# Optimization experiments

Measured on AMD Instinct MI355X. Metric: run time of the kernel, lower is better.

Reference implementation:

```python
import jax, jax.numpy as jnp
import numpy as np

S, T, B = 32, 48, 1024      # src_len, tgt_len, batch
E, H = 256, 1024            # embedding, hidden
VS, VT = 256, 256           # source/target vocab


def setup_inputs() -> dict:
    key = jax.random.key(0)
    ks = jax.random.split(key, 20)
    s = 0.02
    n = jax.random.normal
    inp = {
        "src": jax.random.randint(ks[0], (S, B), 0, VS),
        "tgt": jax.random.randint(ks[1], (T, B), 0, VT),
        "enc_emb": n(ks[2], (VS, E), jnp.float32) * s,
        "enc_Wih0": n(ks[3], (4 * H, E), jnp.float32) * s,
        "enc_Whh0": n(ks[4], (4 * H, H), jnp.float32) * s,
        "enc_b0": jnp.zeros((4 * H,), jnp.float32),
        "enc_Wih1": n(ks[5], (4 * H, H), jnp.float32) * s,
        "enc_Whh1": n(ks[6], (4 * H, H), jnp.float32) * s,
        "enc_b1": jnp.zeros((4 * H,), jnp.float32),
        "dec_emb": n(ks[7], (VT, E), jnp.float32) * s,
        "dec_Wih0": n(ks[8], (4 * H, E), jnp.float32) * s,
        "dec_Whh0": n(ks[9], (4 * H, H), jnp.float32) * s,
        "dec_b0": jnp.zeros((4 * H,), jnp.float32),
        "dec_Wih1": n(ks[10], (4 * H, H), jnp.float32) * s,
        "dec_Whh1": n(ks[11], (4 * H, H), jnp.float32) * s,
        "dec_b1": jnp.zeros((4 * H,), jnp.float32),
        "fc_W": n(ks[12], (H, VT), jnp.float32) * s,
        "fc_b": jnp.zeros((VT,), jnp.float32),
    }
    return inp


def lstm_step(x, h, c, Wih, Whh, b):
    # PyTorch gate order: i, f, g, o
    z = x @ Wih.T + h @ Whh.T + b
    i, f, g, o = jnp.split(z, 4, axis=-1)
    c = jax.nn.sigmoid(f) * c + jax.nn.sigmoid(i) * jnp.tanh(g)
    h = jax.nn.sigmoid(o) * jnp.tanh(c)
    return h, c


def run_layer(xs, Wih, Whh, b):
    # xs: [S, B, in]; returns all hidden states and final (h, c)
    bsz = xs.shape[1]
    h0 = jnp.zeros((bsz, Whh.shape[1]), xs.dtype)

    def step(carry, x):
        h, c = lstm_step(x, carry[0], carry[1], Wih, Whh, b)
        return (h, c), h

    (h, c), hs = jax.lax.scan(step, (h0, h0), xs)
    return hs, h, c


def reference(src, tgt, enc_emb, enc_Wih0, enc_Whh0, enc_b0, enc_Wih1, enc_Whh1,
              enc_b1, dec_emb, dec_Wih0, dec_Whh0, dec_b0, dec_Wih1, dec_Whh1,
              dec_b1, fc_W, fc_b):
    # ---- Encoder: 2-layer LSTM over source ----
    xe = enc_emb[src]                                   # [S, B, E]
    hs0, h0, c0 = run_layer(xe, enc_Wih0, enc_Whh0, enc_b0)
    _, h1, c1 = run_layer(hs0, enc_Wih1, enc_Whh1, enc_b1)

    # ---- Decoder: per-timestep loop, teacher forcing ratio = 1.0 ----
    def dec_step(carry, tok):
        dh0, dc0, dh1, dc1 = carry
        x = dec_emb[tok]                                # [B, E]
        dh0, dc0 = lstm_step(x, dh0, dc0, dec_Wih0, dec_Whh0, dec_b0)
        dh1, dc1 = lstm_step(dh0, dh1, dc1, dec_Wih1, dec_Whh1, dec_b1)
        logits = dh1 @ fc_W + fc_b                      # [B, VT]
        return (dh0, dc0, dh1, dc1), logits

    _, logits = jax.lax.scan(dec_step, (h0, c0, h1, c1), tgt[:-1])  # [T-1, B, VT]
    # outputs[0] is never written in the original -> stays zeros
    out = jnp.concatenate([jnp.zeros((1,) + logits.shape[1:], logits.dtype), logits], axis=0)
    return out
```

## Files before the change

kernel.cpp:

```cpp
#include <hip/hip_runtime.h>
#include <hip/hip_fp16.h>

typedef __attribute__((ext_vector_type(8))) short short8;
typedef __attribute__((ext_vector_type(4))) float floatx4;

#define DEVFN static __device__ __forceinline__

DEVFN short f2h(float v) { return __half_as_short(__float2half(v)); }

DEVFN void gload16(const void* g, void* l) {
  void* gnc = const_cast<void*>(g);
  __builtin_amdgcn_global_load_lds(
      (__attribute__((address_space(1))) void*)gnc,
      (__attribute__((address_space(3))) void*)l, 16, 0, 0);
}

DEVFN unsigned* fset(unsigned* f, int role, int s, int gy) {
  return f + ((((role * 79) + s) * 8 + gy) << 5);
}

__global__ __launch_bounds__(256, 2) void pers_kernel(
    short* xe0, short* xe1, short* xd0, short* xd1,
    const short* wc_e0, const short* wc_e1, const short* wc_d0, const short* wc_d1,
    const float* eb0, const float* eb1, const float* db0, const float* db1,
    const short* embe, const short* embd,
    const int* __restrict__ src, const int* __restrict__ tgt,
    short* dh1, unsigned* flags) {
  __shared__ short smem[32768];
  const int tid = threadIdx.x;
  const int lane = tid & 63;
  const int wv = tid >> 6;
  const int wm = wv >> 1;
  const int wu = wv & 1;
  const int l15 = lane & 15;
  const int l4 = lane >> 4;
  const int bid = blockIdx.x;
  const int xcd = bid & 7;
  const int idx = bid >> 3;
  const int role1 = idx >> 5;
  const int rem = idx & 31;
  const int ut = xcd * 4 + (rem >> 3);
  const int gy = rem & 7;
  const int u0 = ut * 32;
  const int m0 = gy * 128;
  const int srow = lane >> 3;
  const int swseg = ((lane & 7) * 16) ^ (srow * 16);
  const long SL0 = 1024l * 1280, SL1 = 1024l * 2048;

  float cst[16];
#pragma unroll
  for (int i = 0; i < 16; ++i) cst[i] = 0.f;

  for (int s = 0; s < 79; ++s) {
    unsigned* WA = nullptr;
    unsigned* WB = nullptr;
    if (!role1) {
      if (s >= 1) WA = fset(flags, 0, s - 1, gy);
      if (s >= 3) WB = fset(flags, 1, s - 3, gy);
    } else {
      WA = fset(flags, 0, s, gy);
      if (s >= 1) WB = fset(flags, 1, s - 1, gy);
    }
    if (WA || WB) {
      if (tid < 64) {
        unsigned* p = (tid < 32) ? (WA ? WA + tid : nullptr)
                                 : (WB ? WB + (tid - 32) : nullptr);
        if (p) {
          while (__hip_atomic_load(p, __ATOMIC_RELAXED,
                                   __HIP_MEMORY_SCOPE_AGENT) == 0u)
            __builtin_amdgcn_s_sleep(1);
          (void)__hip_atomic_load(p, __ATOMIC_ACQUIRE, __HIP_MEMORY_SCOPE_AGENT);
        }
      }
      __syncthreads();
    }

    const int enc = (s < 32) ? 1 : 0;
    const int t = enc ? s : s - 32;
    const int cur = t % 3, nxt = (t + 1) % 3;
    const short* A; const short* Wt; const float* bs; int ktot;
    short *d1 = nullptr, *d2 = nullptr, *d3 = nullptr, *xq = nullptr;
    int s1 = 0, o1 = 0, xs = 0;
    const short* xe = nullptr; const int* tk = nullptr;
    if (!role1) {
      if (enc) {
        A = xe0 + cur * SL0; Wt = wc_e0; bs = eb0; ktot = 1280;
        d2 = xe1 + cur * SL1;
        s1 = 1280; o1 = 256; xs = 1280;
        if (t < 31) { d1 = xe0 + nxt * SL0; xq = d1; xe = embe; tk = src + (t + 1) * 1024; }
        else        { d1 = xd0;             xq = xd0; xe = embd; tk = tgt; }
      } else {
        A = xd0 + cur * SL0; Wt = wc_d0; bs = db0; ktot = 1280;
        d1 = xd0 + nxt * SL0; s1 = 1280; o1 = 256;
        d2 = xd1 + cur * SL1;
        if (t < 46) { xq = xd0 + nxt * SL0; xs = 1280; xe = embd; tk = tgt + (t + 1) * 1024; }
      }
    } else {
      if (enc) {
        A = xe1 + cur * SL1; Wt = wc_e1; bs = eb1; ktot = 2048;
        d1 = (t < 31) ? (xe1 + nxt * SL1) : xd1; s1 = 2048; o1 = 1024;
      } else {
        A = xd1 + cur * SL1; Wt = wc_d1; bs = db1; ktot = 2048;
        d1 = xd1 + nxt * SL1; s1 = 2048; o1 = 1024;
        d3 = dh1 + (long)t * 1024 * 1024;
      }
    }

    floatx4 acc[4][4];
#pragma unroll
    for (int g = 0; g < 4; ++g)
#pragma unroll
      for (int mi = 0; mi < 4; ++mi) acc[g][mi] = (floatx4){0.f, 0.f, 0.f, 0.f};

    const char* Ab = (const char*)A;
    const char* Wb = (const char*)Wt;
    const long kbytes = (long)ktot * 2;
    const int nkb = ktot >> 6;

    auto stage = [&](int kb, int bufi) {
      const long kboff = (long)kb * 128;
      short* sb = smem + bufi * 16384;
#pragma unroll
      for (int ci = 0; ci < 8; ++ci) {
        const int c = wv * 8 + ci;
        void* lds = (void*)(sb + c * 512);
        if (c < 16) {
          const int row = c * 8 + srow;
          gload16(Ab + (long)(m0 + row) * kbytes + kboff + swseg, lds);
        } else {
          const int cb = c - 16;
          const int wrow = (cb >> 2) * 1024 + u0 + (cb & 3) * 8 + srow;
          gload16(Wb + (long)wrow * kbytes + kboff + swseg, lds);
        }
      }
    };

    stage(0, 0);
    __syncthreads();
    int buf = 0;
    for (int kb = 0; kb < nkb; ++kb) {
      if (kb + 1 < nkb) stage(kb + 1, buf ^ 1);
      const short* sb = smem + buf * 16384;
#pragma unroll
      for (int k0 = 0; k0 < 64; k0 += 32) {
        short8 fa[4];
        short8 fb[4];
#pragma unroll
        for (int mi = 0; mi < 4; ++mi) {
          const int r = wm * 64 + mi * 16 + l15;
          fa[mi] = *(const short8*)(sb + r * 64 + ((k0 + l4 * 8) ^ ((r & 7) << 3)));
        }
        {
          const int r = wu * 16 + l15;
          const int kk = (k0 + l4 * 8) ^ ((r & 7) << 3);
#pragma unroll
          for (int g = 0; g < 4; ++g)
            fb[g] = *(const short8*)(sb + 8192 + (g * 32 + r) * 64 + kk);
        }
#pragma unroll
        for (int g = 0; g < 4; ++g)
#pragma unroll
          for (int mi = 0; mi < 4; ++mi)
            asm volatile("v_mfma_f32_16x16x32_f16 %0, %1, %2, %0"
                         : "+v"(acc[g][mi])
                         : "v"(fa[mi]), "v"(fb[g]));
      }
      __syncthreads();
      buf ^= 1;
    }
    asm volatile("s_nop 7\ns_nop 7\ns_nop 7");

    const int u = u0 + wu * 16 + l15;
    const float bi = bs[u];
    const float bf_ = bs[1024 + u];
    const float bg = bs[2048 + u];
    const float bo = bs[3072 + u];
    short* ht = smem;
    const int uloc = wu * 16 + l15;
#pragma unroll
    for (int mi = 0; mi < 4; ++mi) {
#pragma unroll
      for (int j = 0; j < 4; ++j) {
        const float zi = acc[0][mi][j] + bi;
        const float zf = acc[1][mi][j] + bf_;
        const float zg = acc[2][mi][j] + bg;
        const float zo = acc[3][mi][j] + bo;
        const float gi = 1.f / (1.f + expf(-zi));
        const float gf = 1.f / (1.f + expf(-zf));
        const float gg = tanhf(zg);
        const float go = 1.f / (1.f + expf(-zo));
        const float cn = gf * cst[mi * 4 + j] + gi * gg;
        cst[mi * 4 + j] = cn;
        const int rl = wm * 64 + mi * 16 + l4 * 4 + j;
        ht[rl * 40 + uloc] = f2h(go * tanhf(cn));
      }
    }
    __syncthreads();

    {
      const int rl = tid >> 1;
      const int seg = (tid & 1) * 16;
      const short8 v0 = *(const short8*)(ht + rl * 40 + seg);
      const short8 v1 = *(const short8*)(ht + rl * 40 + seg + 8);
      const long col = u0 + seg;
      if (d1) {
        short* p = d1 + (long)(m0 + rl) * s1 + o1 + col;
        *(short8*)p = v0; *(short8*)(p + 8) = v1;
      }
      if (d2) {
        short* p = d2 + (long)(m0 + rl) * 2048 + col;
        *(short8*)p = v0; *(short8*)(p + 8) = v1;
      }
      if (d3) {
        short* p = d3 + (long)(m0 + rl) * 1024 + col;
        *(short8*)p = v0; *(short8*)(p + 8) = v1;
      }
    }
    if (xq && tid < 128) {
      const int i = ut * 128 + tid;
      const int row = i >> 5;
      const int e8 = (i & 31) * 8;
      const int b = m0 + row;
      const int tok = tk[b];
      const short8 v = *(const short8*)(xe + (long)tok * 256 + e8);
      *(short8*)(xq + (long)b * xs + e8) = v;
    }

    __syncthreads();
    if (tid == 0)
      __hip_atomic_store(fset(flags, role1, s, gy) + ut, 1u,
                         __ATOMIC_RELEASE, __HIP_MEMORY_SCOPE_AGENT);
  }
}

__global__ __launch_bounds__(256) void fc_kernel(
    const short* __restrict__ A, const short* __restrict__ W,
    const float* __restrict__ bias, float* __restrict__ outp) {
  __shared__ short smem[32768];
  const int tid = threadIdx.x;
  const int lane = tid & 63;
  const int wv = tid >> 6;
  const int wm = wv >> 1;
  const int wu = wv & 1;
  const int l15 = lane & 15;
  const int l4 = lane >> 4;
  const int u0 = blockIdx.x * 128;
  const int m0 = blockIdx.y * 128;
  const int srow = lane >> 3;
  const int swseg = ((lane & 7) * 16) ^ (srow * 16);

  floatx4 acc[4][4];
#pragma unroll
  for (int g = 0; g < 4; ++g)
#pragma unroll
    for (int mi = 0; mi < 4; ++mi) acc[g][mi] = (floatx4){0.f, 0.f, 0.f, 0.f};

  const char* Ab = (const char*)A;
  const char* Wb = (const char*)W;
  const long kbytes = 2048;
  const int nkb = 16;

  auto stage = [&](int kb, int bufi) {
    const long kboff = (long)kb * 128;
    short* sb = smem + bufi * 16384;
#pragma unroll
    for (int ci = 0; ci < 8; ++ci) {
      const int c = wv * 8 + ci;
      void* lds = (void*)(sb + c * 512);
      if (c < 16) {
        const int row = c * 8 + srow;
        gload16(Ab + (long)(m0 + row) * kbytes + kboff + swseg, lds);
      } else {
        const int cb = c - 16;
        const int wrow = (cb >> 2) * 32 + u0 + (cb & 3) * 8 + srow;
        gload16(Wb + (long)wrow * kbytes + kboff + swseg, lds);
      }
    }
  };

  stage(0, 0);
  __syncthreads();
  int buf = 0;
  for (int kb = 0; kb < nkb; ++kb) {
    if (kb + 1 < nkb) stage(kb + 1, buf ^ 1);
    const short* sb = smem + buf * 16384;
#pragma unroll
    for (int k0 = 0; k0 < 64; k0 += 32) {
      short8 fa[4];
      short8 fb[4];
#pragma unroll
      for (int mi = 0; mi < 4; ++mi) {
        const int r = wm * 64 + mi * 16 + l15;
        fa[mi] = *(const short8*)(sb + r * 64 + ((k0 + l4 * 8) ^ ((r & 7) << 3)));
      }
      {
        const int r = wu * 16 + l15;
        const int kk = (k0 + l4 * 8) ^ ((r & 7) << 3);
#pragma unroll
        for (int g = 0; g < 4; ++g)
          fb[g] = *(const short8*)(sb + 8192 + (g * 32 + r) * 64 + kk);
      }
#pragma unroll
      for (int g = 0; g < 4; ++g)
#pragma unroll
        for (int mi = 0; mi < 4; ++mi)
          asm volatile("v_mfma_f32_16x16x32_f16 %0, %1, %2, %0"
                       : "+v"(acc[g][mi])
                       : "v"(fa[mi]), "v"(fb[g]));
    }
    __syncthreads();
    buf ^= 1;
  }
  asm volatile("s_nop 7\ns_nop 7\ns_nop 7");

#pragma unroll
  for (int g = 0; g < 4; ++g) {
    const int n = u0 + g * 32 + wu * 16 + l15;
    const float bb = bias[n];
#pragma unroll
    for (int mi = 0; mi < 4; ++mi) {
#pragma unroll
      for (int j = 0; j < 4; ++j) {
        const int r = m0 + wm * 64 + mi * 16 + l4 * 4 + j;
        outp[(long)r * 256 + n] = acc[g][mi][j] + bb;
      }
    }
  }
}

__global__ void wprep(const float* __restrict__ A, const float* __restrict__ B,
                      short* __restrict__ dst, int N, int Ka, int Kb) {
  const int ktot = Ka + Kb;
  const int n8 = ktot >> 3;
  const int total = N * n8;
  for (int idx = blockIdx.x * 256 + threadIdx.x; idx < total; idx += gridDim.x * 256) {
    const int n = idx / n8;
    const int k = (idx - n * n8) * 8;
    const float* s = (k < Ka) ? (A + (long)n * Ka + k) : (B + (long)n * Kb + (k - Ka));
    short8 v;
#pragma unroll
    for (int j = 0; j < 8; ++j) v[j] = f2h(s[j]);
    *(short8*)(dst + (long)n * ktot + k) = v;
  }
}

__global__ void embprep(const float* __restrict__ s, short* __restrict__ d, int total8) {
  const int idx = blockIdx.x * 256 + threadIdx.x;
  if (idx >= total8) return;
  short8 v;
#pragma unroll
  for (int j = 0; j < 8; ++j) v[j] = f2h(s[idx * 8 + j]);
  *(short8*)(d + idx * 8) = v;
}

__global__ void fcwprep(const float* __restrict__ fcW, short* __restrict__ dst) {
  const int idx = blockIdx.x * 256 + threadIdx.x;
  const int v = idx & 255;
  const int h = (idx >> 8) * 8;
  short8 o;
#pragma unroll
  for (int j = 0; j < 8; ++j) o[j] = f2h(fcW[(long)(h + j) * 256 + v]);
  *(short8*)(dst + (long)v * 1024 + h) = o;
}

__global__ void initk(const int* __restrict__ src, const float* __restrict__ emb,
                      short* __restrict__ xe0, short* __restrict__ xe1) {
  const int idx = blockIdx.x * 256 + threadIdx.x;
  if (idx < 1024 * 160) {
    const int b = idx / 160;
    const int k = (idx - b * 160) * 8;
    short8 v;
    if (k < 256) {
      const int tok = src[b];
#pragma unroll
      for (int j = 0; j < 8; ++j) v[j] = f2h(emb[(long)tok * 256 + k + j]);
    } else {
#pragma unroll
      for (int j = 0; j < 8; ++j) v[j] = 0;
    }
    *(short8*)(xe0 + (long)b * 1280 + k) = v;
  } else {
    const int i = idx - 1024 * 160;
    if (i < 1024 * 128) {
      const int b = i >> 7;
      const int k = 1024 + (i & 127) * 8;
      short8 v;
#pragma unroll
      for (int j = 0; j < 8; ++j) v[j] = 0;
      *(short8*)(xe1 + (long)b * 2048 + k) = v;
    }
  }
}

extern "C" void kernel_launch(void* const* d_in, const int* in_sizes, int n_in,
                              void* d_out, int out_size, void* d_ws, size_t ws_size,
                              hipStream_t stream) {
  (void)in_sizes; (void)n_in; (void)out_size; (void)ws_size;
  const int* src = (const int*)d_in[0];
  const int* tgt = (const int*)d_in[1];
  const float* enc_emb = (const float*)d_in[2];
  const float* eW0i = (const float*)d_in[3];
  const float* eW0h = (const float*)d_in[4];
  const float* eb0 = (const float*)d_in[5];
  const float* eW1i = (const float*)d_in[6];
  const float* eW1h = (const float*)d_in[7];
  const float* eb1 = (const float*)d_in[8];
  const float* dec_emb = (const float*)d_in[9];
  const float* dW0i = (const float*)d_in[10];
  const float* dW0h = (const float*)d_in[11];
  const float* db0 = (const float*)d_in[12];
  const float* dW1i = (const float*)d_in[13];
  const float* dW1h = (const float*)d_in[14];
  const float* db1 = (const float*)d_in[15];
  const float* fcW = (const float*)d_in[16];
  const float* fcb = (const float*)d_in[17];
  float* out = (float*)d_out;

  char* ws = (char*)d_ws;
  size_t off = 0;
  auto carve = [&](size_t bytes) {
    void* p = ws + off;
    off += (bytes + 255) & ~(size_t)255;
    return p;
  };
  short* wc_e0 = (short*)carve(4096l * 1280 * 2);
  short* wc_e1 = (short*)carve(4096l * 2048 * 2);
  short* wc_d0 = (short*)carve(4096l * 1280 * 2);
  short* wc_d1 = (short*)carve(4096l * 2048 * 2);
  short* fcwt = (short*)carve(256l * 1024 * 2);
  short* embe = (short*)carve(256l * 256 * 2);
  short* embd = (short*)carve(256l * 256 * 2);
  short* xe0 = (short*)carve(3l * 1024 * 1280 * 2);
  short* xe1 = (short*)carve(3l * 1024 * 2048 * 2);
  short* xd0 = (short*)carve(3l * 1024 * 1280 * 2);
  short* xd1 = (short*)carve(3l * 1024 * 2048 * 2);
  short* dh1 = (short*)carve(47l * 1024 * 1024 * 2);
  const size_t flagbytes = 2l * 79 * 8 * 32 * 4;
  unsigned* flags = (unsigned*)carve(flagbytes);

  hipMemsetAsync(flags, 0, flagbytes, stream);
  hipMemsetAsync(out, 0, 1024l * 256 * 4, stream);

  wprep<<<2560, 256, 0, stream>>>(eW0i, eW0h, wc_e0, 4096, 256, 1024);
  wprep<<<4096, 256, 0, stream>>>(eW1i, eW1h, wc_e1, 4096, 1024, 1024);
  wprep<<<2560, 256, 0, stream>>>(dW0i, dW0h, wc_d0, 4096, 256, 1024);
  wprep<<<4096, 256, 0, stream>>>(dW1i, dW1h, wc_d1, 4096, 1024, 1024);
  embprep<<<32, 256, 0, stream>>>(enc_emb, embe, 8192);
  embprep<<<32, 256, 0, stream>>>(dec_emb, embd, 8192);
  fcwprep<<<128, 256, 0, stream>>>(fcW, fcwt);
  initk<<<1152, 256, 0, stream>>>(src, enc_emb, xe0, xe1);

  pers_kernel<<<512, 256, 0, stream>>>(
      xe0, xe1, xd0, xd1, wc_e0, wc_e1, wc_d0, wc_d1,
      eb0, eb1, db0, db1, embe, embd, src, tgt, dh1, flags);

  fc_kernel<<<dim3(2, 376), 256, 0, stream>>>(dh1, fcwt, fcb, out + 1024l * 256);
}
```

Before: 4.207 ms.

## Widen persistent LSTM blocks to 64 units with triple-buffered LDS pipeline

Each persistent workgroup now has 512 threads and covers 64 hidden units instead of 32, so 256 blocks replace 512 and the flag arrays shrink. The K loop moves from double to triple buffering, with explicit vmcnt waits and raw barriers so global-to-LDS loads two stages ahead overlap the MFMA work. Dynamic LDS grows to 144 KB, which limits occupancy to one block per CU and leaves fewer blocks to cover the CUs. The aim is to halve the A-tile reloads per unit and the synchronisation traffic, at the cost of less parallelism per timestep.

```diff
diff --git a/kernel.cpp b/kernel.cpp
--- a/kernel.cpp
+++ b/kernel.cpp
@@ -16,32 +16,32 @@
 }
 
 DEVFN unsigned* fset(unsigned* f, int role, int s, int gy) {
-  return f + ((((role * 79) + s) * 8 + gy) << 5);
-}
-
-__global__ __launch_bounds__(256, 2) void pers_kernel(
+  return f + ((((role * 79) + s) * 8 + gy) << 4);
+}
+
+__global__ __launch_bounds__(512, 2) void pers_kernel(
     short* xe0, short* xe1, short* xd0, short* xd1,
     const short* wc_e0, const short* wc_e1, const short* wc_d0, const short* wc_d1,
     const float* eb0, const float* eb1, const float* db0, const float* db1,
     const short* embe, const short* embd,
     const int* __restrict__ src, const int* __restrict__ tgt,
     short* dh1, unsigned* flags) {
-  __shared__ short smem[32768];
+  extern __shared__ short smem[];
   const int tid = threadIdx.x;
   const int lane = tid & 63;
   const int wv = tid >> 6;
-  const int wm = wv >> 1;
-  const int wu = wv & 1;
+  const int wm = wv >> 2;
+  const int wu = wv & 3;
   const int l15 = lane & 15;
   const int l4 = lane >> 4;
   const int bid = blockIdx.x;
   const int xcd = bid & 7;
   const int idx = bid >> 3;
-  const int role1 = idx >> 5;
-  const int rem = idx & 31;
-  const int ut = xcd * 4 + (rem >> 3);
+  const int role1 = idx >> 4;
+  const int rem = idx & 15;
+  const int ut4 = xcd * 2 + (rem >> 3);
   const int gy = rem & 7;
-  const int u0 = ut * 32;
+  const int u0 = ut4 * 64;
   const int m0 = gy * 128;
   const int srow = lane >> 3;
   const int swseg = ((lane & 7) * 16) ^ (srow * 16);
@@ -62,9 +62,9 @@
       if (s >= 1) WB = fset(flags, 1, s - 1, gy);
     }
     if (WA || WB) {
-      if (tid < 64) {
-        unsigned* p = (tid < 32) ? (WA ? WA + tid : nullptr)
-                                 : (WB ? WB + (tid - 32) : nullptr);
+      if (tid < 32) {
+        unsigned* p = (tid < 16) ? (WA ? WA + tid : nullptr)
+                                 : (WB ? WB + (tid - 16) : nullptr);
         if (p) {
           while (__hip_atomic_load(p, __ATOMIC_RELAXED,
                                    __HIP_MEMORY_SCOPE_AGENT) == 0u)
@@ -119,28 +119,35 @@
 
     auto stage = [&](int kb, int bufi) {
       const long kboff = (long)kb * 128;
-      short* sb = smem + bufi * 16384;
-#pragma unroll
-      for (int ci = 0; ci < 8; ++ci) {
-        const int c = wv * 8 + ci;
-        void* lds = (void*)(sb + c * 512);
+      short* sb = smem + bufi * 24576;
+#pragma unroll
+      for (int ci = 0; ci < 6; ++ci) {
+        const int c = wv * 6 + ci;
         if (c < 16) {
           const int row = c * 8 + srow;
-          gload16(Ab + (long)(m0 + row) * kbytes + kboff + swseg, lds);
+          gload16(Ab + (long)(m0 + row) * kbytes + kboff + swseg, sb + c * 512);
         } else {
-          const int cb = c - 16;
-          const int wrow = (cb >> 2) * 1024 + u0 + (cb & 3) * 8 + srow;
-          gload16(Wb + (long)wrow * kbytes + kboff + swseg, lds);
+          const int cw = c - 16;
+          const int wr = cw * 8 + srow;
+          const int wrow = (wr >> 6) * 1024 + u0 + (wr & 63);
+          gload16(Wb + (long)wrow * kbytes + kboff + swseg,
+                  sb + 8192 + cw * 512);
         }
       }
     };
 
+    asm volatile("s_waitcnt vmcnt(0)" ::: "memory");
     stage(0, 0);
-    __syncthreads();
-    int buf = 0;
+    stage(1, 1);
     for (int kb = 0; kb < nkb; ++kb) {
-      if (kb + 1 < nkb) stage(kb + 1, buf ^ 1);
-      const short* sb = smem + buf * 16384;
+      if (kb + 1 < nkb)  asm volatile("s_waitcnt vmcnt(6)" ::: "memory");
+      else               asm volatile("s_waitcnt vmcnt(0)" ::: "memory");
+      __builtin_amdgcn_sched_barrier(0);
+      __builtin_amdgcn_s_barrier();
+      __builtin_amdgcn_sched_barrier(0);
+      if (kb + 2 < nkb) stage(kb + 2, (kb + 2) % 3);
+      __builtin_amdgcn_sched_barrier(0);
+      const short* sb = smem + (kb % 3) * 24576;
 #pragma unroll
       for (int k0 = 0; k0 < 64; k0 += 32) {
         short8 fa[4];
@@ -150,12 +157,11 @@
           const int r = wm * 64 + mi * 16 + l15;
           fa[mi] = *(const short8*)(sb + r * 64 + ((k0 + l4 * 8) ^ ((r & 7) << 3)));
         }
-        {
-          const int r = wu * 16 + l15;
-          const int kk = (k0 + l4 * 8) ^ ((r & 7) << 3);
-#pragma unroll
-          for (int g = 0; g < 4; ++g)
-            fb[g] = *(const short8*)(sb + 8192 + (g * 32 + r) * 64 + kk);
+#pragma unroll
+        for (int g = 0; g < 4; ++g) {
+          const int r = g * 64 + wu * 16 + l15;
+          fb[g] = *(const short8*)(sb + 8192 + r * 64 +
+                                   ((k0 + l4 * 8) ^ ((r & 7) << 3)));
         }
 #pragma unroll
         for (int g = 0; g < 4; ++g)
@@ -165,9 +171,8 @@
                          : "+v"(acc[g][mi])
                          : "v"(fa[mi]), "v"(fb[g]));
       }
-      __syncthreads();
-      buf ^= 1;
-    }
+    }
+    __syncthreads();
     asm volatile("s_nop 7\ns_nop 7\ns_nop 7");
 
     const int u = u0 + wu * 16 + l15;
@@ -192,16 +197,16 @@
         const float cn = gf * cst[mi * 4 + j] + gi * gg;
         cst[mi * 4 + j] = cn;
         const int rl = wm * 64 + mi * 16 + l4 * 4 + j;
-        ht[rl * 40 + uloc] = f2h(go * tanhf(cn));
+        ht[rl * 72 + uloc] = f2h(go * tanhf(cn));
       }
     }
     __syncthreads();
 
     {
-      const int rl = tid >> 1;
-      const int seg = (tid & 1) * 16;
-      const short8 v0 = *(const short8*)(ht + rl * 40 + seg);
-      const short8 v1 = *(const short8*)(ht + rl * 40 + seg + 8);
+      const int rl = tid >> 2;
+      const int seg = (tid & 3) * 16;
+      const short8 v0 = *(const short8*)(ht + rl * 72 + seg);
+      const short8 v1 = *(const short8*)(ht + rl * 72 + seg + 8);
       const long col = u0 + seg;
       if (d1) {
         short* p = d1 + (long)(m0 + rl) * s1 + o1 + col;
@@ -216,8 +221,8 @@
         *(short8*)p = v0; *(short8*)(p + 8) = v1;
       }
     }
-    if (xq && tid < 128) {
-      const int i = ut * 128 + tid;
+    if (xq && tid < 256) {
+      const int i = ut4 * 256 + tid;
       const int row = i >> 5;
       const int e8 = (i & 31) * 8;
       const int b = m0 + row;
@@ -228,7 +233,7 @@
 
     __syncthreads();
     if (tid == 0)
-      __hip_atomic_store(fset(flags, role1, s, gy) + ut, 1u,
+      __hip_atomic_store(fset(flags, role1, s, gy) + ut4, 1u,
                          __ATOMIC_RELEASE, __HIP_MEMORY_SCOPE_AGENT);
   }
 }
@@ -435,7 +440,7 @@
   short* xd0 = (short*)carve(3l * 1024 * 1280 * 2);
   short* xd1 = (short*)carve(3l * 1024 * 2048 * 2);
   short* dh1 = (short*)carve(47l * 1024 * 1024 * 2);
-  const size_t flagbytes = 2l * 79 * 8 * 32 * 4;
+  const size_t flagbytes = 2l * 79 * 8 * 16 * 4;
   unsigned* flags = (unsigned*)carve(flagbytes);
 
   hipMemsetAsync(flags, 0, flagbytes, stream);
@@ -450,7 +455,13 @@
   fcwprep<<<128, 256, 0, stream>>>(fcW, fcwt);
   initk<<<1152, 256, 0, stream>>>(src, enc_emb, xe0, xe1);
 
-  pers_kernel<<<512, 256, 0, stream>>>(
+  static bool attr_set = false;
+  if (!attr_set) {
+    hipFuncSetAttribute((const void*)pers_kernel,
+                        hipFuncAttributeMaxDynamicSharedMemorySize, 147456);
+    attr_set = true;
+  }
+  pers_kernel<<<256, 512, 147456, stream>>>(
       xe0, xe1, xd0, xd1, wc_e0, wc_e1, wc_d0, wc_d1,
       eb0, eb1, db0, db1, embe, embd, src, tgt, dh1, flags);
 
```

Measured after the change: 3.791 ms. -9.9%, faster.
